# Kernel tuning notes

Hardware: AMD Instinct MI355X
Metric: run time of the kernel (lower is better)

## Reference

```python
import jax, jax.numpy as jnp
import numpy as np

B, D, L, NH = 8, 1024, 1024, 8
DK = D // NH  # = Dv = 128
NEG = -1e30


def setup_inputs() -> dict:
    key = jax.random.key(0)
    kx, km, kq, kk, kv, ko = jax.random.split(key, 6)
    x = jax.random.normal(kx, (B, D, L), dtype=jnp.float32)
    # binary mask over sequence positions (float, as in the torch code)
    mask = (jax.random.uniform(km, (B, L)) > 0.1).astype(jnp.float32)
    # xavier-ish scale for per-head projections, kaiming-ish for Wo
    s_qkv = np.sqrt(2.0 / (D + DK)).astype(np.float32)
    Wq = jax.random.normal(kq, (NH, D, DK), dtype=jnp.float32) * s_qkv
    Wk = jax.random.normal(kk, (NH, D, DK), dtype=jnp.float32) * s_qkv
    Wv = jax.random.normal(kv, (NH, D, DK), dtype=jnp.float32) * s_qkv
    Wo = jax.random.normal(ko, (D, DK * NH), dtype=jnp.float32) * np.sqrt(2.0 / D).astype(np.float32)
    return {"x": x, "mask": mask, "Wq": Wq, "Wk": Wk, "Wv": Wv, "Wo": Wo}


def reference(x, mask, Wq, Wk, Wv, Wo):
    # x: [B, D, L] -> [B, L, D]
    xt = jnp.swapaxes(x, 1, 2)
    scale = 1.0 / np.sqrt(DK).astype(np.float32)
    # batched per-head projections (equivalent to the per-head loop)
    q = jnp.einsum("bld,hdk->bhlk", xt, Wq)  # [B,H,L,Dk]
    k = jnp.einsum("bld,hdk->bhlk", xt, Wk)
    v = jnp.einsum("bld,hdk->bhlk", xt, Wv)
    # scores[b,h,q_pos,k_pos]
    scores = jnp.einsum("bhqd,bhkd->bhqk", q, k) * scale
    # mask.unsqueeze(2) in torch -> additive mask along the QUERY axis
    scores = scores + (1.0 - mask)[:, None, :, None] * NEG
    # faithful quirk: softmax over dim=1 of [B,Lq,Lk] == query axis (axis=2 here)
    attn = jax.nn.softmax(scores, axis=2)
    heads = jnp.einsum("bhqk,bhkd->bhqd", attn, v)  # [B,H,L,Dv]
    head = jnp.swapaxes(heads, 1, 2).reshape(B, L, NH * DK)  # concat heads
    out = head @ Wo  # [B, L, D]
    return jnp.swapaxes(out, 1, 2)  # [B, D, L]
```

## Files before the change

### kernel.cpp

```cpp
#include <hip/hip_runtime.h>

typedef short bf16x8 __attribute__((ext_vector_type(8)));
typedef float f32x4 __attribute__((ext_vector_type(4)));
typedef unsigned short u16x8 __attribute__((ext_vector_type(8)));

#define MASK_NEG (-1e30f)

__device__ __forceinline__ unsigned short f2bf(float f) {
  union { float f; unsigned u; } v; v.f = f;
  unsigned r = v.u + 0x7fffu + ((v.u >> 16) & 1u);
  return (unsigned short)(r >> 16);
}

__device__ __forceinline__ float bf2f(unsigned short u) {
  union { unsigned u; float f; } v; v.u = ((unsigned)u) << 16;
  return v.f;
}

__device__ __forceinline__ void gl_lds16(const void* g, void* l) {
  __builtin_amdgcn_global_load_lds(
      (__attribute__((address_space(1))) void*)(void*)g,
      (__attribute__((address_space(3))) void*)l, 16, 0, 0);
}

__device__ __forceinline__ void transpose_tile(
    const float* __restrict__ s, unsigned short* __restrict__ d,
    int R, int C, int x0, int y0, int t, float tile[64][65]) {
  {
    const int r = t >> 4, c4 = (t & 15) * 4;
    for (int it = 0; it < 4; ++it) {
      const int rr = r + it * 16;
      const float4 v = *(const float4*)(s + (size_t)(y0 + rr) * C + x0 + c4);
      tile[rr][c4 + 0] = v.x; tile[rr][c4 + 1] = v.y;
      tile[rr][c4 + 2] = v.z; tile[rr][c4 + 3] = v.w;
    }
  }
  __syncthreads();
  {
    const int cc = t >> 4, r4 = (t & 15) * 4;
    for (int it = 0; it < 4; ++it) {
      const int c = cc + it * 16;
      ushort4 o;
      o.x = f2bf(tile[r4 + 0][c]); o.y = f2bf(tile[r4 + 1][c]);
      o.z = f2bf(tile[r4 + 2][c]); o.w = f2bf(tile[r4 + 3][c]);
      *(ushort4*)(d + (size_t)(x0 + c) * R + y0 + r4) = o;
    }
  }
}

__global__ __launch_bounds__(256) void transpose_x_wo(
    const float* __restrict__ x, const float* __restrict__ Wo,
    unsigned short* __restrict__ xt, unsigned short* __restrict__ Wot) {
  __shared__ float tile[64][65];
  const int z = blockIdx.z;
  const float* s = (z < 8) ? (x + (size_t)z * 1048576) : Wo;
  unsigned short* d = (z < 8) ? (xt + (size_t)z * 1048576) : Wot;
  transpose_tile(s, d, 1024, 1024, blockIdx.x * 64, blockIdx.y * 64,
                 threadIdx.x, tile);
}

__global__ __launch_bounds__(256) void transpose_w24(
    const float* __restrict__ Wq, const float* __restrict__ Wk,
    const float* __restrict__ Wv, unsigned short* __restrict__ WqkvT) {
  __shared__ float tile[64][65];
  const int z = blockIdx.z;
  const int sel = z >> 3, h = z & 7;
  const float* base = (sel == 0) ? Wq : (sel == 1) ? Wk : Wv;
  const float* s = base + (size_t)h * 131072;
  unsigned short* d = WqkvT + (size_t)z * 131072;
  transpose_tile(s, d, 1024, 128, blockIdx.x * 64, blockIdx.y * 64,
                 threadIdx.x, tile);
}

template<bool F32OUT>
__global__ __launch_bounds__(256) void gemm_tn(
    const unsigned short* __restrict__ A, const unsigned short* __restrict__ B,
    void* __restrict__ Cv,
    int K, int ldA, int ldB, int ldC, float scale,
    long sAl, long sAb, long sAh,
    long sBl, long sBb, long sBh,
    long sCl, long sCb, long sCh,
    int zbase, int zdiv)
{
  __shared__ unsigned short As[128 * 64];
  __shared__ unsigned short Bs[128 * 64];
  const int z = blockIdx.z;
  const int g = zbase + z;
  const int gb = g / zdiv, gh = g % zdiv;
  const unsigned short* Ab = A + (size_t)z * sAl + (size_t)gb * sAb + (size_t)gh * sAh;
  const unsigned short* Bb = B + (size_t)z * sBl + (size_t)gb * sBb + (size_t)gh * sBh;
  const int m0 = blockIdx.y * 128, n0 = blockIdx.x * 128;
  const int t = threadIdx.x;
  const int lane = t & 63;
  const int wave = t >> 6;
  const int wm = wave >> 1, wn = wave & 1;

  const int sr2 = t >> 3;
  const int ss8 = t & 7;
  const int sq8 = ss8 ^ (sr2 & 7);

  const unsigned short* ap0 = Ab + (size_t)(m0 +  0 + sr2) * ldA + sq8 * 8;
  const unsigned short* ap1 = Ab + (size_t)(m0 + 32 + sr2) * ldA + sq8 * 8;
  const unsigned short* ap2 = Ab + (size_t)(m0 + 64 + sr2) * ldA + sq8 * 8;
  const unsigned short* ap3 = Ab + (size_t)(m0 + 96 + sr2) * ldA + sq8 * 8;
  const unsigned short* bp0 = Bb + (size_t)(n0 +  0 + sr2) * ldB + sq8 * 8;
  const unsigned short* bp1 = Bb + (size_t)(n0 + 32 + sr2) * ldB + sq8 * 8;
  const unsigned short* bp2 = Bb + (size_t)(n0 + 64 + sr2) * ldB + sq8 * 8;
  const unsigned short* bp3 = Bb + (size_t)(n0 + 96 + sr2) * ldB + sq8 * 8;

  char* asd0 = (char*)As +     0 + t * 16;
  char* asd1 = (char*)As +  4096 + t * 16;
  char* asd2 = (char*)As +  8192 + t * 16;
  char* asd3 = (char*)As + 12288 + t * 16;
  char* bsd0 = (char*)Bs +     0 + t * 16;
  char* bsd1 = (char*)Bs +  4096 + t * 16;
  char* bsd2 = (char*)Bs +  8192 + t * 16;
  char* bsd3 = (char*)Bs + 12288 + t * 16;

  const int tq = lane & 15, qd = lane >> 4;

  f32x4 acc[4][4];
  #pragma unroll
  for (int i = 0; i < 4; ++i)
    #pragma unroll
    for (int j = 0; j < 4; ++j)
      acc[i][j] = f32x4{0.f, 0.f, 0.f, 0.f};

  const int kIters = K >> 6;
  for (int kt = 0; kt < kIters; ++kt) {
    __syncthreads();
    gl_lds16(ap0, asd0); gl_lds16(ap1, asd1);
    gl_lds16(ap2, asd2); gl_lds16(ap3, asd3);
    gl_lds16(bp0, bsd0); gl_lds16(bp1, bsd1);
    gl_lds16(bp2, bsd2); gl_lds16(bp3, bsd3);
    ap0 += 64; ap1 += 64; ap2 += 64; ap3 += 64;
    bp0 += 64; bp1 += 64; bp2 += 64; bp3 += 64;
    __builtin_amdgcn_s_waitcnt(0x0f70);
    __syncthreads();

    #pragma unroll
    for (int kk = 0; kk < 2; ++kk) {
      bf16x8 af[4], bfr[4];
      #pragma unroll
      for (int i = 0; i < 4; ++i) {
        const int R = wm * 64 + i * 16 + tq;
        const int slot = (kk * 4 + qd) ^ (R & 7);
        af[i] = *(const bf16x8*)(As + R * 64 + slot * 8);
      }
      #pragma unroll
      for (int j = 0; j < 4; ++j) {
        const int R = wn * 64 + j * 16 + tq;
        const int slot = (kk * 4 + qd) ^ (R & 7);
        bfr[j] = *(const bf16x8*)(Bs + R * 64 + slot * 8);
      }
      #pragma unroll
      for (int i = 0; i < 4; ++i)
        #pragma unroll
        for (int j = 0; j < 4; ++j)
          acc[i][j] = __builtin_amdgcn_mfma_f32_16x16x32_bf16(af[i], bfr[j], acc[i][j], 0, 0, 0);
    }
  }

  const size_t cOff = (size_t)z * sCl + (size_t)gb * sCb + (size_t)gh * sCh;
  #pragma unroll
  for (int i = 0; i < 4; ++i) {
    const int row = m0 + wm * 64 + i * 16 + qd * 4;
    #pragma unroll
    for (int j = 0; j < 4; ++j) {
      const int col = n0 + wn * 64 + j * 16 + tq;
      if constexpr (F32OUT) {
        float* C = (float*)Cv + cOff;
        #pragma unroll
        for (int rr = 0; rr < 4; ++rr)
          C[(size_t)(row + rr) * ldC + col] = acc[i][j][rr] * scale;
      } else {
        unsigned short* C = (unsigned short*)Cv + cOff;
        #pragma unroll
        for (int rr = 0; rr < 4; ++rr)
          C[(size_t)(row + rr) * ldC + col] = f2bf(acc[i][j][rr] * scale);
      }
    }
  }
}

__global__ __launch_bounds__(256) void gemm_scores_fused(
    const unsigned short* __restrict__ QKV,
    unsigned short* __restrict__ E, float* __restrict__ colsum,
    const float* __restrict__ mask, int zbase)
{
  __shared__ unsigned short sbuf[32768];
  unsigned short* As = sbuf;
  unsigned short* Bs = sbuf + 16384;
  const int z = blockIdx.z;
  const int g = zbase + z;
  const int b = g >> 3, h = g & 7;
  const unsigned short* Ab = QKV + (size_t)b * 3145728 + (size_t)h * 131072;
  const unsigned short* Bb = Ab + 1048576;
  const int m0 = blockIdx.y * 128, n0 = blockIdx.x * 128;
  const int t = threadIdx.x;
  const int lane = t & 63;
  const int wave = t >> 6;
  const int wm = wave >> 1, wn = wave & 1;
  const int tq = lane & 15, qd = lane >> 4;

  const unsigned short* Aq = Ab + (size_t)m0 * 128;
  const unsigned short* Bk = Bb + (size_t)n0 * 128;
  #pragma unroll
  for (int it = 0; it < 8; ++it) {
    const int c = it * 256 + t;
    const int row = c >> 4;
    const int src = (c ^ (c >> 4)) & 15;
    gl_lds16(Aq + (size_t)row * 128 + src * 8, (char*)As + c * 16);
    gl_lds16(Bk + (size_t)row * 128 + src * 8, (char*)Bs + c * 16);
  }
  __builtin_amdgcn_s_waitcnt(0x0f70);
  __syncthreads();

  f32x4 acc[4][4];
  #pragma unroll
  for (int i = 0; i < 4; ++i)
    #pragma unroll
    for (int j = 0; j < 4; ++j)
      acc[i][j] = f32x4{0.f, 0.f, 0.f, 0.f};

  #pragma unroll
  for (int kk = 0; kk < 4; ++kk) {
    bf16x8 af[4], bfr[4];
    #pragma unroll
    for (int i = 0; i < 4; ++i) {
      const int R = wm * 64 + i * 16 + tq;
      const int slot = (kk * 4 + qd) ^ (R & 15);
      af[i] = *(const bf16x8*)(As + R * 128 + slot * 8);
    }
    #pragma unroll
    for (int j = 0; j < 4; ++j) {
      const int R = wn * 64 + j * 16 + tq;
      const int slot = (kk * 4 + qd) ^ (R & 15);
      bfr[j] = *(const bf16x8*)(Bs + R * 128 + slot * 8);
    }
    #pragma unroll
    for (int i = 0; i < 4; ++i)
      #pragma unroll
      for (int j = 0; j < 4; ++j)
        acc[i][j] = __builtin_amdgcn_mfma_f32_16x16x32_bf16(af[i], bfr[j], acc[i][j], 0, 0, 0);
  }

  __syncthreads();

  unsigned short* T = sbuf;
  float* cs = colsum + (size_t)g * 1024;
  const float scl = 0.08838834764831845f;
  const float* mrow = mask + (size_t)b * 1024;

  float cp[4] = {0.f, 0.f, 0.f, 0.f};
  #pragma unroll
  for (int i = 0; i < 4; ++i) {
    const int r0 = wm * 64 + i * 16 + qd * 4;
    const float4 m4 = *(const float4*)(mrow + m0 + r0);
    const float aq[4] = {(1.f - m4.x) * MASK_NEG - 20.f, (1.f - m4.y) * MASK_NEG - 20.f,
                         (1.f - m4.z) * MASK_NEG - 20.f, (1.f - m4.w) * MASK_NEG - 20.f};
    #pragma unroll
    for (int rr = 0; rr < 4; ++rr) {
      #pragma unroll
      for (int j = 0; j < 4; ++j) {
        const int cl = wn * 64 + j * 16 + tq;
        const float e = __expf(acc[i][j][rr] * scl + aq[rr]);
        cp[j] += e;
        T[(r0 + rr) * 136 + cl] = f2bf(e);
      }
    }
  }
  #pragma unroll
  for (int j = 0; j < 4; ++j) {
    float v = cp[j];
    v += __shfl_xor(v, 16, 64);
    v += __shfl_xor(v, 32, 64);
    if (qd == 0)
      atomicAdd(&cs[n0 + wn * 64 + j * 16 + tq], v);
  }
  __syncthreads();

  unsigned short* Ep = E + (size_t)z * 1048576 + (size_t)m0 * 1024 + n0;
  #pragma unroll
  for (int r = 0; r < 8; ++r) {
    const int c = r * 256 + t;
    const int row = c >> 4, sl = c & 15;
    u16x8 v = *(const u16x8*)(T + row * 136 + sl * 8);
    *(u16x8*)(Ep + (size_t)row * 1024 + sl * 8) = v;
  }
}

__global__ __launch_bounds__(256) void tvscale(
    const unsigned short* __restrict__ QKV, unsigned short* __restrict__ Vp,
    const float* __restrict__ colsum, int zbase)
{
  __shared__ unsigned short tile[64][72];
  const int z = blockIdx.z;
  const int g = zbase + z;
  const int b = g >> 3, h = g & 7;
  const unsigned short* S = QKV + (size_t)b * 3145728 + (size_t)(16 + h) * 131072;
  unsigned short* D = Vp + (size_t)g * 131072;
  const float* cs = colsum + (size_t)g * 1024;
  const int l0 = blockIdx.x * 64;
  const int d0 = blockIdx.y * 64;
  const int t = threadIdx.x;
  {
    const int r = t >> 4, c4 = (t & 15) * 4;
    for (int it = 0; it < 4; ++it) {
      const int rr = r + it * 16;
      const ushort4 v = *(const ushort4*)(S + (size_t)(l0 + rr) * 128 + d0 + c4);
      *(ushort4*)&tile[rr][c4] = v;
    }
  }
  __syncthreads();
  {
    const int cc = t >> 4, r4 = (t & 15) * 4;
    const float4 c4v = *(const float4*)(cs + l0 + r4);
    for (int it = 0; it < 4; ++it) {
      const int c = cc + it * 16;
      ushort4 o;
      o.x = f2bf(bf2f(tile[r4 + 0][c]) / c4v.x);
      o.y = f2bf(bf2f(tile[r4 + 1][c]) / c4v.y);
      o.z = f2bf(bf2f(tile[r4 + 2][c]) / c4v.z);
      o.w = f2bf(bf2f(tile[r4 + 3][c]) / c4v.w);
      *(ushort4*)(D + (size_t)(d0 + c) * 1024 + l0 + r4) = o;
    }
  }
}

extern "C" void kernel_launch(void* const* d_in, const int* in_sizes, int n_in,
                              void* d_out, int out_size, void* d_ws, size_t ws_size,
                              hipStream_t stream) {
  const float* x    = (const float*)d_in[0];
  const float* mask = (const float*)d_in[1];
  const float* Wq   = (const float*)d_in[2];
  const float* Wk   = (const float*)d_in[3];
  const float* Wv   = (const float*)d_in[4];
  const float* Wo   = (const float*)d_in[5];
  float* out = (float*)d_out;

  char* p = (char*)d_ws;
  unsigned short* xt    = (unsigned short*)p; p += 16777216;
  unsigned short* WqkvT = (unsigned short*)p; p += 6291456;
  unsigned short* Wot   = (unsigned short*)p; p += 2097152;
  unsigned short* QKV   = (unsigned short*)p; p += 50331648;
  unsigned short* Vp    = (unsigned short*)p; p += 16777216;
  unsigned short* Hp    = (unsigned short*)p; p += 16777216;
  float* colsum = (float*)p; p += 262144;
  const size_t fixedBytes = (size_t)(p - (char*)d_ws);

  long nbh = 1;
  if (ws_size > fixedBytes) {
    nbh = (long)((ws_size - fixedBytes) / 2097152);
    if (nbh < 1) nbh = 1;
    if (nbh > 64) nbh = 64;
  }
  unsigned short* Ep = (unsigned short*)p;

  hipMemsetAsync(colsum, 0, 262144, stream);

  transpose_x_wo<<<dim3(16, 16, 9), 256, 0, stream>>>(x, Wo, xt, Wot);
  transpose_w24<<<dim3(2, 16, 24), 256, 0, stream>>>(Wq, Wk, Wv, WqkvT);

  gemm_tn<false><<<dim3(1, 8, 192), 256, 0, stream>>>(
      xt, WqkvT, (void*)QKV, 1024, 1024, 1024, 128, 1.f,
      0L, 1048576L, 0L,  0L, 0L, 131072L,  0L, 3145728L, 131072L, 0, 24);

  for (int s0 = 0; s0 < 64; s0 += (int)nbh) {
    const int cnt = (int)(((64 - s0) < nbh) ? (64 - s0) : nbh);
    gemm_scores_fused<<<dim3(8, 8, cnt), 256, 0, stream>>>(QKV, Ep, colsum, mask, s0);
    tvscale<<<dim3(16, 2, cnt), 256, 0, stream>>>(QKV, Vp, colsum, s0);
    gemm_tn<false><<<dim3(1, 8, cnt), 256, 0, stream>>>(
        Ep, Vp, (void*)Hp, 1024, 1024, 1024, 1024, 1.f,
        1048576L, 0L, 0L,  0L, 1048576L, 131072L,  0L, 1048576L, 128L, s0, 8);
  }
  gemm_tn<true><<<dim3(8, 8, 8), 256, 0, stream>>>(
      Wot, Hp, (void*)out, 1024, 1024, 1024, 1024, 1.f,
      0L, 0L, 0L,  0L, 1048576L, 0L,  0L, 1048576L, 0L, 0, 1);
}
```

Before: 297.3 us.

## Fuse QK exp and PV into flash-style kernel, drop materialized exp matrix

The score kernel now only accumulates column sums of exp(scores) and no longer writes the full bf16 exp matrix E. A new fused kernel recomputes QK^T per 64-key tile, applies exp and the mask, stages P in LDS and multiplies it by the column-normalized V, writing the head outputs directly. This removes the large E write/read and the batched loop, at the cost of computing QK^T twice. Workgroup indices are also remapped (XCD-style swizzle) in the GEMMs for cache locality.

```diff
diff --git a/kernel.cpp b/kernel.cpp
--- a/kernel.cpp
+++ b/kernel.cpp
@@ -2,7 +2,6 @@
 
 typedef short bf16x8 __attribute__((ext_vector_type(8)));
 typedef float f32x4 __attribute__((ext_vector_type(4)));
-typedef unsigned short u16x8 __attribute__((ext_vector_type(8)));
 
 #define MASK_NEG (-1e30f)
 
@@ -84,12 +83,21 @@
 {
   __shared__ unsigned short As[128 * 64];
   __shared__ unsigned short Bs[128 * 64];
-  const int z = blockIdx.z;
+  int bx, by, bz;
+  {
+    const int nx = gridDim.x, ny = gridDim.y;
+    const int nwg = nx * ny * gridDim.z;
+    int flat = blockIdx.x + nx * (blockIdx.y + ny * blockIdx.z);
+    if ((nwg & 7) == 0) flat = (flat & 7) * (nwg >> 3) + (flat >> 3);
+    bx = flat % nx; flat /= nx;
+    by = flat % ny; bz = flat / ny;
+  }
+  const int z = bz;
   const int g = zbase + z;
   const int gb = g / zdiv, gh = g % zdiv;
   const unsigned short* Ab = A + (size_t)z * sAl + (size_t)gb * sAb + (size_t)gh * sAh;
   const unsigned short* Bb = B + (size_t)z * sBl + (size_t)gb * sBb + (size_t)gh * sBh;
-  const int m0 = blockIdx.y * 128, n0 = blockIdx.x * 128;
+  const int m0 = by * 128, n0 = bx * 128;
   const int t = threadIdx.x;
   const int lane = t & 63;
   const int wave = t >> 6;
@@ -183,20 +191,20 @@
   }
 }
 
-__global__ __launch_bounds__(256) void gemm_scores_fused(
-    const unsigned short* __restrict__ QKV,
-    unsigned short* __restrict__ E, float* __restrict__ colsum,
-    const float* __restrict__ mask, int zbase)
+__global__ __launch_bounds__(256) void gemm_scores_colsum(
+    const unsigned short* __restrict__ QKV, float* __restrict__ colsum,
+    const float* __restrict__ mask)
 {
   __shared__ unsigned short sbuf[32768];
   unsigned short* As = sbuf;
   unsigned short* Bs = sbuf + 16384;
-  const int z = blockIdx.z;
-  const int g = zbase + z;
+  int flat = blockIdx.x + 8 * (blockIdx.y + 8 * blockIdx.z);
+  flat = (flat & 7) * 512 + (flat >> 3);
+  const int bx = flat & 7, by = (flat >> 3) & 7, g = flat >> 6;
   const int b = g >> 3, h = g & 7;
   const unsigned short* Ab = QKV + (size_t)b * 3145728 + (size_t)h * 131072;
   const unsigned short* Bb = Ab + 1048576;
-  const int m0 = blockIdx.y * 128, n0 = blockIdx.x * 128;
+  const int m0 = by * 128, n0 = bx * 128;
   const int t = threadIdx.x;
   const int lane = t & 63;
   const int wave = t >> 6;
@@ -245,9 +253,6 @@
         acc[i][j] = __builtin_amdgcn_mfma_f32_16x16x32_bf16(af[i], bfr[j], acc[i][j], 0, 0, 0);
   }
 
-  __syncthreads();
-
-  unsigned short* T = sbuf;
   float* cs = colsum + (size_t)g * 1024;
   const float scl = 0.08838834764831845f;
   const float* mrow = mask + (size_t)b * 1024;
@@ -263,10 +268,8 @@
     for (int rr = 0; rr < 4; ++rr) {
       #pragma unroll
       for (int j = 0; j < 4; ++j) {
-        const int cl = wn * 64 + j * 16 + tq;
         const float e = __expf(acc[i][j][rr] * scl + aq[rr]);
         cp[j] += e;
-        T[(r0 + rr) * 136 + cl] = f2bf(e);
       }
     }
   }
@@ -278,25 +281,14 @@
     if (qd == 0)
       atomicAdd(&cs[n0 + wn * 64 + j * 16 + tq], v);
   }
-  __syncthreads();
-
-  unsigned short* Ep = E + (size_t)z * 1048576 + (size_t)m0 * 1024 + n0;
-  #pragma unroll
-  for (int r = 0; r < 8; ++r) {
-    const int c = r * 256 + t;
-    const int row = c >> 4, sl = c & 15;
-    u16x8 v = *(const u16x8*)(T + row * 136 + sl * 8);
-    *(u16x8*)(Ep + (size_t)row * 1024 + sl * 8) = v;
-  }
 }
 
 __global__ __launch_bounds__(256) void tvscale(
     const unsigned short* __restrict__ QKV, unsigned short* __restrict__ Vp,
-    const float* __restrict__ colsum, int zbase)
+    const float* __restrict__ colsum)
 {
   __shared__ unsigned short tile[64][72];
-  const int z = blockIdx.z;
-  const int g = zbase + z;
+  const int g = blockIdx.z;
   const int b = g >> 3, h = g & 7;
   const unsigned short* S = QKV + (size_t)b * 3145728 + (size_t)(16 + h) * 131072;
   unsigned short* D = Vp + (size_t)g * 131072;
@@ -328,6 +320,162 @@
   }
 }
 
+__global__ __launch_bounds__(256, 2) void attn_pv_fused(
+    const unsigned short* __restrict__ QKV, const unsigned short* __restrict__ Vp,
+    unsigned short* __restrict__ Hp, const float* __restrict__ mask)
+{
+  __shared__ unsigned short lds[32768];
+  unsigned short* Qs = lds;
+  unsigned short* Ps = lds;
+  unsigned short* Ks = lds + 16384;
+  unsigned short* Vs = lds + 24576;
+
+  const int bid = blockIdx.x;
+  const int w = ((bid & 7) << 6) | (bid >> 3);
+  const int g = w >> 3, qx = w & 7;
+  const int b = g >> 3, h = g & 7;
+  const unsigned short* Qg = QKV + (size_t)b * 3145728 + (size_t)h * 131072
+                                 + (size_t)qx * 16384;
+  const unsigned short* Kg = QKV + (size_t)b * 3145728 + (size_t)(8 + h) * 131072;
+  const unsigned short* Vg = Vp + (size_t)g * 131072;
+
+  const int t = threadIdx.x;
+  const int lane = t & 63, wave = t >> 6;
+  const int wm = wave >> 1, wn = wave & 1;
+  const int tq = lane & 15, qd = lane >> 4;
+
+  #pragma unroll
+  for (int it = 0; it < 8; ++it) {
+    const int c = it * 256 + t;
+    const int row = c >> 4;
+    const int src = (c ^ (c >> 4)) & 15;
+    gl_lds16(Qg + (size_t)row * 128 + src * 8, (char*)Qs + c * 16);
+  }
+  __builtin_amdgcn_s_waitcnt(0x0f70);
+  __syncthreads();
+
+  bf16x8 qf[4][4];
+  #pragma unroll
+  for (int i = 0; i < 4; ++i) {
+    const int R = wm * 64 + i * 16 + tq;
+    #pragma unroll
+    for (int kk = 0; kk < 4; ++kk)
+      qf[i][kk] = *(const bf16x8*)(Qs + R * 128 + (((kk * 4 + qd) ^ (R & 15)) * 8));
+  }
+  __syncthreads();
+
+  f32x4 acc_h[4][4];
+  #pragma unroll
+  for (int i = 0; i < 4; ++i)
+    #pragma unroll
+    for (int j = 0; j < 4; ++j)
+      acc_h[i][j] = f32x4{0.f, 0.f, 0.f, 0.f};
+
+  const float scl = 0.08838834764831845f;
+  float aq[4][4];
+  {
+    const float* mrow = mask + (size_t)b * 1024 + qx * 128;
+    #pragma unroll
+    for (int i = 0; i < 4; ++i) {
+      const float4 m4 = *(const float4*)(mrow + wm * 64 + i * 16 + qd * 4);
+      aq[i][0] = (1.f - m4.x) * MASK_NEG - 20.f;
+      aq[i][1] = (1.f - m4.y) * MASK_NEG - 20.f;
+      aq[i][2] = (1.f - m4.z) * MASK_NEG - 20.f;
+      aq[i][3] = (1.f - m4.w) * MASK_NEG - 20.f;
+    }
+  }
+
+  for (int kt = 0; kt < 16; ++kt) {
+    __syncthreads();
+    #pragma unroll
+    for (int it = 0; it < 4; ++it) {
+      const int c = it * 256 + t;
+      const int row = c >> 4;
+      const int src = (c ^ (c >> 4)) & 15;
+      gl_lds16(Kg + (size_t)(kt * 64 + row) * 128 + src * 8, (char*)Ks + c * 16);
+    }
+    #pragma unroll
+    for (int it = 0; it < 4; ++it) {
+      const int c = it * 256 + t;
+      const int row = c >> 3;
+      const int src = (c ^ (c >> 3)) & 7;
+      gl_lds16(Vg + (size_t)row * 1024 + kt * 64 + src * 8, (char*)Vs + c * 16);
+    }
+    __builtin_amdgcn_s_waitcnt(0x0f70);
+    __syncthreads();
+
+    f32x4 acc_s[4][2];
+    #pragma unroll
+    for (int i = 0; i < 4; ++i)
+      #pragma unroll
+      for (int j = 0; j < 2; ++j)
+        acc_s[i][j] = f32x4{0.f, 0.f, 0.f, 0.f};
+    #pragma unroll
+    for (int kk = 0; kk < 4; ++kk) {
+      bf16x8 kf[2];
+      #pragma unroll
+      for (int j = 0; j < 2; ++j) {
+        const int R = wn * 32 + j * 16 + tq;
+        kf[j] = *(const bf16x8*)(Ks + R * 128 + (((kk * 4 + qd) ^ (R & 15)) * 8));
+      }
+      #pragma unroll
+      for (int i = 0; i < 4; ++i)
+        #pragma unroll
+        for (int j = 0; j < 2; ++j)
+          acc_s[i][j] = __builtin_amdgcn_mfma_f32_16x16x32_bf16(qf[i][kk], kf[j], acc_s[i][j], 0, 0, 0);
+    }
+
+    #pragma unroll
+    for (int i = 0; i < 4; ++i) {
+      const int q0 = wm * 64 + i * 16 + qd * 4;
+      #pragma unroll
+      for (int rr = 0; rr < 4; ++rr) {
+        const int q = q0 + rr;
+        #pragma unroll
+        for (int j = 0; j < 2; ++j) {
+          const int kl = wn * 32 + j * 16 + tq;
+          const float e = __expf(acc_s[i][j][rr] * scl + aq[i][rr]);
+          Ps[q * 64 + ((((kl >> 3) ^ (q & 7)) * 8) | (kl & 7))] = f2bf(e);
+        }
+      }
+    }
+    __syncthreads();
+
+    #pragma unroll
+    for (int k2 = 0; k2 < 2; ++k2) {
+      bf16x8 pf[4], vf[4];
+      #pragma unroll
+      for (int i = 0; i < 4; ++i) {
+        const int R = wm * 64 + i * 16 + tq;
+        pf[i] = *(const bf16x8*)(Ps + R * 64 + (((k2 * 4 + qd) ^ (R & 7)) * 8));
+      }
+      #pragma unroll
+      for (int j = 0; j < 4; ++j) {
+        const int R = wn * 64 + j * 16 + tq;
+        vf[j] = *(const bf16x8*)(Vs + R * 64 + (((k2 * 4 + qd) ^ (R & 7)) * 8));
+      }
+      #pragma unroll
+      for (int i = 0; i < 4; ++i)
+        #pragma unroll
+        for (int j = 0; j < 4; ++j)
+          acc_h[i][j] = __builtin_amdgcn_mfma_f32_16x16x32_bf16(pf[i], vf[j], acc_h[i][j], 0, 0, 0);
+    }
+  }
+
+  unsigned short* Hb = Hp + (size_t)b * 1048576 + (size_t)qx * 131072 + h * 128;
+  #pragma unroll
+  for (int i = 0; i < 4; ++i) {
+    const int q0 = wm * 64 + i * 16 + qd * 4;
+    #pragma unroll
+    for (int j = 0; j < 4; ++j) {
+      const int dv = wn * 64 + j * 16 + tq;
+      #pragma unroll
+      for (int rr = 0; rr < 4; ++rr)
+        Hb[(size_t)(q0 + rr) * 1024 + dv] = f2bf(acc_h[i][j][rr]);
+    }
+  }
+}
+
 extern "C" void kernel_launch(void* const* d_in, const int* in_sizes, int n_in,
                               void* d_out, int out_size, void* d_ws, size_t ws_size,
                               hipStream_t stream) {
@@ -347,15 +495,6 @@
   unsigned short* Vp    = (unsigned short*)p; p += 16777216;
   unsigned short* Hp    = (unsigned short*)p; p += 16777216;
   float* colsum = (float*)p; p += 262144;
-  const size_t fixedBytes = (size_t)(p - (char*)d_ws);
-
-  long nbh = 1;
-  if (ws_size > fixedBytes) {
-    nbh = (long)((ws_size - fixedBytes) / 2097152);
-    if (nbh < 1) nbh = 1;
-    if (nbh > 64) nbh = 64;
-  }
-  unsigned short* Ep = (unsigned short*)p;
 
   hipMemsetAsync(colsum, 0, 262144, stream);
 
@@ -366,14 +505,12 @@
       xt, WqkvT, (void*)QKV, 1024, 1024, 1024, 128, 1.f,
       0L, 1048576L, 0L,  0L, 0L, 131072L,  0L, 3145728L, 131072L, 0, 24);
 
-  for (int s0 = 0; s0 < 64; s0 += (int)nbh) {
-    const int cnt = (int)(((64 - s0) < nbh) ? (64 - s0) : nbh);
-    gemm_scores_fused<<<dim3(8, 8, cnt), 256, 0, stream>>>(QKV, Ep, colsum, mask, s0);
-    tvscale<<<dim3(16, 2, cnt), 256, 0, stream>>>(QKV, Vp, colsum, s0);
-    gemm_tn<false><<<dim3(1, 8, cnt), 256, 0, stream>>>(
-        Ep, Vp, (void*)Hp, 1024, 1024, 1024, 1024, 1.f,
-        1048576L, 0L, 0L,  0L, 1048576L, 131072L,  0L, 1048576L, 128L, s0, 8);
-  }
+  gemm_scores_colsum<<<dim3(8, 8, 64), 256, 0, stream>>>(QKV, colsum, mask);
+
+  tvscale<<<dim3(16, 2, 64), 256, 0, stream>>>(QKV, Vp, colsum);
+
+  attn_pv_fused<<<dim3(512, 1, 1), 256, 0, stream>>>(QKV, Vp, Hp, mask);
+
   gemm_tn<true><<<dim3(8, 8, 8), 256, 0, stream>>>(
       Wot, Hp, (void*)out, 1024, 1024, 1024, 1024, 1.f,
       0L, 0L, 0L,  0L, 1048576L, 0L,  0L, 1048576L, 0L, 0, 1);
```

Result: faster. 276.2 us (-7.1%).
